# Kernel optimization log

Hardware: AMD Instinct MI355X
Metric: run time of the kernel (lower is better)

The kernel has to match this reference:

```python
import jax, jax.numpy as jnp
import numpy as np

B, N, DIM, H = 4, 2048, 256, 8
HD = DIM // H  # head_dim = 32
N_LAYERS = 2


def quantum_map(x):
    # cat over last dim: [cos(x+i*pi/2), sin(x+i*pi/2)] for i in 0..n_layers-1
    feats = []
    for i in range(N_LAYERS):
        phase = x + i * (np.pi / 2)
        feats.append(jnp.cos(phase))
        feats.append(jnp.sin(phase))
    return jnp.concatenate(feats, axis=-1)  # [..., 4*HD]


def setup_inputs() -> dict:
    key = jax.random.key(0)
    ks = jax.random.split(key, 10)
    s = 1.0 / np.sqrt(DIM)
    return {
        "x": jax.random.normal(ks[0], (B, N, DIM), dtype=jnp.float32),
        "topo_weights": jax.random.uniform(ks[1], (B, N, N), dtype=jnp.float32),
        "Wq": jax.random.normal(ks[2], (DIM, DIM), dtype=jnp.float32) * s,
        "bq": jnp.zeros((DIM,), jnp.float32),
        "Wk": jax.random.normal(ks[3], (DIM, DIM), dtype=jnp.float32) * s,
        "bk": jnp.zeros((DIM,), jnp.float32),
        "Wv": jax.random.normal(ks[4], (DIM, DIM), dtype=jnp.float32) * s,
        "bv": jnp.zeros((DIM,), jnp.float32),
        "Wo": jax.random.normal(ks[5], (DIM, DIM), dtype=jnp.float32) * s,
        "bo": jnp.zeros((DIM,), jnp.float32),
    }


def reference(x, topo_weights, Wq, bq, Wk, bk, Wv, bv, Wo, bo):
    b, n, c = x.shape
    q = (x @ Wq + bq).reshape(b, n, H, HD)
    k = (x @ Wk + bk).reshape(b, n, H, HD)
    v = (x @ Wv + bv).reshape(b, n, H, HD)
    q = quantum_map(q)  # [b,n,H,4*HD]
    k = quantum_map(k)
    scores = jnp.einsum('bnhd,bmhd->bnmh', q, k) / np.sqrt(HD)
    scores = scores * topo_weights[..., None]  # [b,n,m,h]
    attn = jax.nn.softmax(scores, axis=2)
    out = jnp.einsum('bnmh,bmhd->bnhd', attn, v).reshape(b, n, c)
    return out @ Wo + bo
```

## Files before the change

### kernel.cpp

```cpp
#include <hip/hip_runtime.h>
#include <math.h>

#define Bn 4
#define Nn 2048
#define Hn 8
#define HDn 32
#define Dn 256
#define MHALF 1024
#define NT 64

typedef _Float16 h1;
typedef __attribute__((ext_vector_type(2))) _Float16 h2;
typedef __attribute__((ext_vector_type(8))) _Float16 h8;
typedef __attribute__((ext_vector_type(4))) float fx4;

#define QSCALE 0.35355339059327373f
#define QS_L2E 0.5101185553493001f
#define SH_L2E 5.770780163555851f

__global__ __launch_bounds__(256) void cvtW_kernel(
    const float* __restrict__ Wq, const float* __restrict__ Wk,
    const float* __restrict__ Wv, const float* __restrict__ Wo,
    h1* __restrict__ WT)
{
    __shared__ float tw[64][65];
    const int w = blockIdx.z;
    const int d0 = blockIdx.y * 64, o0 = blockIdx.x * 64;
    const float* W = (w == 0) ? Wq : (w == 1) ? Wk : (w == 2) ? Wv : Wo;
    const int rr = threadIdx.x >> 6, cc = threadIdx.x & 63;
#pragma unroll
    for (int i = 0; i < 16; ++i)
        tw[rr + i * 4][cc] = W[(size_t)(d0 + rr + i * 4) * 256 + o0 + cc];
    __syncthreads();
#pragma unroll
    for (int i = 0; i < 16; ++i) {
        const int row = rr + i * 4;
        WT[(size_t)w * 65536 + (size_t)(o0 + row) * 256 + d0 + cc] = (h1)tw[cc][row];
    }
}

__global__ __launch_bounds__(256) __attribute__((amdgpu_waves_per_eu(4, 4)))
void proj_kernel(
    const float* __restrict__ x, const h1* __restrict__ WT,
    const float* __restrict__ bq, const float* __restrict__ bk,
    const float* __restrict__ bv,
    h1* __restrict__ fq, h1* __restrict__ fk, h1* __restrict__ vT)
{
    __shared__ __align__(16) h1 fbuf[64][264];
    const int tid = threadIdx.x;
    const int w = tid >> 6;
    const int lane = tid & 63;
    const int quad = lane >> 4;
    const int l15 = lane & 15;
    const int wsel = blockIdx.y >> 1;
    const int hg = blockIdx.y & 1;
    const int r0 = blockIdx.x * 64;
    const int arow = r0 + w * 16 + l15;
    const int b = r0 >> 11, n0 = r0 & (Nn - 1);

    const h1* WTw = WT + (size_t)wsel * 65536;
    fx4 acc[8];
#pragma unroll
    for (int ct = 0; ct < 8; ++ct) acc[ct] = (fx4){0.f, 0.f, 0.f, 0.f};

    for (int ks = 0; ks < 8; ++ks) {
        float xv[8];
        *(float4*)&xv[0] = *(const float4*)&x[(size_t)arow * 256 + ks * 32 + quad * 8];
        *(float4*)&xv[4] = *(const float4*)&x[(size_t)arow * 256 + ks * 32 + quad * 8 + 4];
        h8 Ahi, Alo;
#pragma unroll
        for (int j = 0; j < 8; ++j) {
            const h1 hi = (h1)xv[j];
            Ahi[j] = hi;
            Alo[j] = (h1)(xv[j] - (float)hi);
        }
        h8 Bf[8];
#pragma unroll
        for (int ct = 0; ct < 8; ++ct)
            Bf[ct] = *(const h8*)&WTw[(size_t)(hg * 128 + ct * 16 + l15) * 256 + ks * 32 + quad * 8];
#pragma unroll
        for (int ct = 0; ct < 8; ++ct) {
            acc[ct] = __builtin_amdgcn_mfma_f32_16x16x32_f16(Ahi, Bf[ct], acc[ct], 0, 0, 0);
            acc[ct] = __builtin_amdgcn_mfma_f32_16x16x32_f16(Alo, Bf[ct], acc[ct], 0, 0, 0);
        }
    }

    const float* bias = (wsel == 0) ? bq : (wsel == 1) ? bk : bv;

    if (wsel < 2) {
        h1* f = (wsel == 0) ? fq : fk;
#pragma unroll
        for (int ct = 0; ct < 8; ++ct) {
            const int c = ct * 16 + l15;
            const float bb = bias[hg * 128 + c];
            const int hh4 = c >> 5, dd = c & 31;
#pragma unroll
            for (int r = 0; r < 4; ++r) {
                const float val = acc[ct][r] + bb;
                const float sv = __sinf(val), cv = __cosf(val);
                h1* fp = &fbuf[w * 16 + quad * 4 + r][hh4 * 64 + dd];
                fp[0]  = (h1)cv;
                fp[32] = (h1)sv;
            }
        }
        __syncthreads();
        const int row = tid >> 2, q4 = tid & 3;
#pragma unroll
        for (int g = 0; g < 8; ++g) {
            const int chunk = q4 + g * 4;
            const int hh4 = chunk >> 3, within = chunk & 7;
            const h8 val = *(const h8*)&fbuf[row][hh4 * 64 + within * 8];
            const int head = hg * 4 + hh4;
            *(h8*)&f[((size_t)(b * Hn + head) * Nn + n0 + row) * 64 + within * 8] = val;
        }
    } else {
        h1 (*vst)[132] = (h1(*)[132])fbuf;
#pragma unroll
        for (int ct = 0; ct < 8; ++ct) {
            const int c = ct * 16 + l15;
            const float bb = bias[hg * 128 + c];
#pragma unroll
            for (int r = 0; r < 4; ++r)
                vst[w * 16 + quad * 4 + r][c] = (h1)(acc[ct][r] + bb);
        }
        __syncthreads();
        const int c2 = tid & 127, half = tid >> 7;
        const int head = hg * 4 + (c2 >> 5), dd = c2 & 31;
        h1* vp = vT + ((size_t)((b * Hn + head) * HDn + dd)) * Nn + n0;
#pragma unroll
        for (int g = 0; g < 4; ++g) {
            const int gg = half * 4 + g;
            h8 pk;
#pragma unroll
            for (int j = 0; j < 8; ++j) {
                const int zz = gg * 8 + j;
                const int blk = zz >> 5, z = zz & 31;
                const int src = blk * 32 + ((z & 7) >> 2) * 16 + (z >> 3) * 4 + (z & 3);
                pk[j] = vst[src][c2];
            }
            *(h8*)(vp + gg * 8) = pk;
        }
    }
}

__global__ __launch_bounds__(512, 1) void attn_kernel(
    const h1* __restrict__ fq, const h1* __restrict__ fk, const h1* __restrict__ vT,
    const float* __restrict__ topo, float* __restrict__ pacc, float* __restrict__ pl)
{
    __shared__ __align__(16) float tbuf[2][NT][40];

    const int b = blockIdx.y;
    const int mh = blockIdx.z;
    const int n0 = blockIdx.x * NT;
    const int tid = threadIdx.x;
    const int w = tid >> 6;
    const int h = w;
    const int lane = tid & 63;
    const int quad = lane >> 4;
    const int l15 = lane & 15;

    const h1* qfh = fq + (size_t)(b * Hn + h) * Nn * 64;
    const h1* kfh = fk + (size_t)(b * Hn + h) * Nn * 64;
    const h1* vTh = vT + (size_t)(b * Hn + h) * HDn * Nn;

    const int trow = tid >> 3, tcol4 = (tid & 7) * 4;
    const float* tpg = topo + (size_t)b * Nn * Nn + (size_t)(n0 + trow) * Nn + tcol4;

    h8 qfr[4][2];
#pragma unroll
    for (int qs = 0; qs < 4; ++qs)
#pragma unroll
        for (int ks = 0; ks < 2; ++ks)
            qfr[qs][ks] = *(const h8*)(qfh + (size_t)(n0 + qs * 16 + l15) * 64 + ks * 32 + quad * 8);

    fx4 acc[4][2];
    float lsum[4];
#pragma unroll
    for (int qs = 0; qs < 4; ++qs) {
#pragma unroll
        for (int ds = 0; ds < 2; ++ds) acc[qs][ds] = (fx4){0.f, 0.f, 0.f, 0.f};
        lsum[qs] = 0.f;
    }

    const int mbase = mh * MHALF;
    const fx4 z4 = {0.f, 0.f, 0.f, 0.f};

    float4 rt = *(const float4*)(tpg + mbase);

    for (int it = 0; it < MHALF / 32; ++it) {
        const int m0 = mbase + it * 32;
        const int cur = it & 1;

        h8 kfr[2][2];
#pragma unroll
        for (int ms = 0; ms < 2; ++ms)
#pragma unroll
            for (int ks = 0; ks < 2; ++ks)
                kfr[ms][ks] = *(const h8*)(kfh + (size_t)(m0 + ms * 16 + l15) * 64 + ks * 32 + quad * 8);
        h8 bV[2];
#pragma unroll
        for (int ds = 0; ds < 2; ++ds)
            bV[ds] = *(const h8*)(vTh + (size_t)(ds * 16 + l15) * Nn + m0 + quad * 8);

        *(float4*)&tbuf[cur][trow][tcol4] = rt;
        if (it < MHALF / 32 - 1) rt = *(const float4*)(tpg + m0 + 32);
        __asm__ volatile("s_waitcnt lgkmcnt(0)\n\ts_barrier" ::: "memory");

#pragma unroll
        for (int qs = 0; qs < 4; ++qs) {
            h2 pk[2][2];
#pragma unroll
            for (int ms = 0; ms < 2; ++ms) {
                fx4 tmp = __builtin_amdgcn_mfma_f32_16x16x32_f16(kfr[ms][0], qfr[qs][0], z4, 0, 0, 0);
                fx4 S2  = __builtin_amdgcn_mfma_f32_16x16x32_f16(kfr[ms][1], qfr[qs][1], tmp, 0, 0, 0);
                const fx4 tv = *(const fx4*)&tbuf[cur][qs * 16 + l15][ms * 16 + quad * 4];
                const float p0 = exp2f(fmaf(S2[0] * tv[0], QS_L2E, -SH_L2E));
                const float p1 = exp2f(fmaf(S2[1] * tv[1], QS_L2E, -SH_L2E));
                const float p2 = exp2f(fmaf(S2[2] * tv[2], QS_L2E, -SH_L2E));
                const float p3 = exp2f(fmaf(S2[3] * tv[3], QS_L2E, -SH_L2E));
                lsum[qs] += (p0 + p1) + (p2 + p3);
                pk[ms][0] = __builtin_bit_cast(h2, __builtin_amdgcn_cvt_pkrtz(p0, p1));
                pk[ms][1] = __builtin_bit_cast(h2, __builtin_amdgcn_cvt_pkrtz(p2, p3));
            }
            union { h8 v; h2 p[4]; } pa;
            pa.p[0] = pk[0][0]; pa.p[1] = pk[0][1];
            pa.p[2] = pk[1][0]; pa.p[3] = pk[1][1];
#pragma unroll
            for (int ds = 0; ds < 2; ++ds)
                acc[qs][ds] = __builtin_amdgcn_mfma_f32_16x16x32_f16(pa.v, bV[ds], acc[qs][ds], 0, 0, 0);
        }
    }

#pragma unroll
    for (int qs = 0; qs < 4; ++qs) {
        lsum[qs] += __shfl_xor(lsum[qs], 16);
        lsum[qs] += __shfl_xor(lsum[qs], 32);
    }

    float* paccm = pacc + (size_t)mh * Bn * Nn * Dn;
    float* plm   = pl   + (size_t)mh * Bn * Nn * Hn;
#pragma unroll
    for (int qs = 0; qs < 4; ++qs) {
#pragma unroll
        for (int r = 0; r < 4; ++r) {
            const size_t grow = (size_t)b * Nn + n0 + qs * 16 + quad * 4 + r;
            paccm[grow * Dn + h * HDn + l15]      = acc[qs][0][r];
            paccm[grow * Dn + h * HDn + 16 + l15] = acc[qs][1][r];
        }
        if (quad == 0)
            plm[((size_t)b * Nn + n0 + qs * 16 + l15) * Hn + h] = lsum[qs];
    }
}

__global__ __launch_bounds__(256) void oproj_kernel(
    const float* __restrict__ pacc, const float* __restrict__ pl,
    const h1* __restrict__ WoT, const float* __restrict__ bo,
    float* __restrict__ out)
{
    const int tid = threadIdx.x;
    const int w = tid >> 6;
    const int lane = tid & 63;
    const int quad = lane >> 4;
    const int l15 = lane & 15;
    const int r0 = blockIdx.x * 64;
    const int hg = blockIdx.y;
    const int arow = r0 + w * 16 + l15;
    const size_t PACC = (size_t)Bn * Nn * Dn;
    const size_t PL = (size_t)Bn * Nn * Hn;

    float rl[8];
#pragma unroll
    for (int hh = 0; hh < 8; ++hh) {
        const float l = pl[(size_t)arow * Hn + hh] + pl[PL + (size_t)arow * Hn + hh];
        rl[hh] = __builtin_amdgcn_rcpf(l);
    }

    fx4 acc[8];
#pragma unroll
    for (int ct = 0; ct < 8; ++ct) acc[ct] = (fx4){0.f, 0.f, 0.f, 0.f};

    for (int ks = 0; ks < 8; ++ks) {
        float a0[8], a1[8];
        const size_t base = (size_t)arow * Dn + ks * 32 + quad * 8;
        *(float4*)&a0[0] = *(const float4*)&pacc[base];
        *(float4*)&a0[4] = *(const float4*)&pacc[base + 4];
        *(float4*)&a1[0] = *(const float4*)&pacc[PACC + base];
        *(float4*)&a1[4] = *(const float4*)&pacc[PACC + base + 4];
        h8 Ahi, Alo;
#pragma unroll
        for (int j = 0; j < 8; ++j) {
            const float yv = (a0[j] + a1[j]) * rl[ks];
            const h1 hi = (h1)yv;
            Ahi[j] = hi;
            Alo[j] = (h1)(yv - (float)hi);
        }
        h8 Bf[8];
#pragma unroll
        for (int ct = 0; ct < 8; ++ct)
            Bf[ct] = *(const h8*)&WoT[(size_t)(hg * 128 + ct * 16 + l15) * 256 + ks * 32 + quad * 8];
#pragma unroll
        for (int ct = 0; ct < 8; ++ct) {
            acc[ct] = __builtin_amdgcn_mfma_f32_16x16x32_f16(Ahi, Bf[ct], acc[ct], 0, 0, 0);
            acc[ct] = __builtin_amdgcn_mfma_f32_16x16x32_f16(Alo, Bf[ct], acc[ct], 0, 0, 0);
        }
    }

#pragma unroll
    for (int ct = 0; ct < 8; ++ct) {
        const int col = hg * 128 + ct * 16 + l15;
        const float bb = bo[col];
#pragma unroll
        for (int r = 0; r < 4; ++r)
            out[(size_t)(r0 + w * 16 + quad * 4 + r) * 256 + col] = acc[ct][r] + bb;
    }
}

extern "C" void kernel_launch(void* const* d_in, const int* in_sizes, int n_in,
                              void* d_out, int out_size, void* d_ws, size_t ws_size,
                              hipStream_t stream)
{
    const float* x    = (const float*)d_in[0];
    const float* topo = (const float*)d_in[1];
    const float* Wq   = (const float*)d_in[2];
    const float* bq   = (const float*)d_in[3];
    const float* Wk   = (const float*)d_in[4];
    const float* bk   = (const float*)d_in[5];
    const float* Wv   = (const float*)d_in[6];
    const float* bv   = (const float*)d_in[7];
    const float* Wo   = (const float*)d_in[8];
    const float* bo   = (const float*)d_in[9];
    float* out = (float*)d_out;

    char* ws = (char*)d_ws;
    const size_t MB = 1024 * 1024;
    h1* WT = (h1*)ws;
    h1* fq = (h1*)(ws + 1 * MB);
    h1* fk = (h1*)(ws + 9 * MB);
    h1* vT = (h1*)(ws + 17 * MB);
    float* pacc = (float*)(ws + 21 * MB);
    float* pl   = (float*)(ws + 37 * MB);

    cvtW_kernel<<<dim3(4, 4, 4), 256, 0, stream>>>(Wq, Wk, Wv, Wo, WT);
    proj_kernel<<<dim3(128, 6), 256, 0, stream>>>(x, WT, bq, bk, bv, fq, fk, vT);
    attn_kernel<<<dim3(Nn / NT, Bn, 2), 512, 0, stream>>>(fq, fk, vT, topo, pacc, pl);
    oproj_kernel<<<dim3(128, 2), 256, 0, stream>>>(pacc, pl, WT + 3 * 65536, bo, out);
}
```

Before: 212.9 us.

## Split attention key range into four chunks and fold score scale into topo

Measured after the change: 232.7 us. 9.3% more time.

```diff
diff --git a/kernel.cpp b/kernel.cpp
--- a/kernel.cpp
+++ b/kernel.cpp
@@ -6,7 +6,7 @@
 #define Hn 8
 #define HDn 32
 #define Dn 256
-#define MHALF 1024
+#define MQ 512
 #define NT 64
 
 typedef _Float16 h1;
@@ -143,7 +143,7 @@
     }
 }
 
-__global__ __launch_bounds__(512, 1) void attn_kernel(
+__global__ __launch_bounds__(512, 2) void attn_kernel(
     const h1* __restrict__ fq, const h1* __restrict__ fk, const h1* __restrict__ vT,
     const float* __restrict__ topo, float* __restrict__ pacc, float* __restrict__ pl)
 {
@@ -182,12 +182,12 @@
         lsum[qs] = 0.f;
     }
 
-    const int mbase = mh * MHALF;
+    const int mbase = mh * MQ;
     const fx4 z4 = {0.f, 0.f, 0.f, 0.f};
 
     float4 rt = *(const float4*)(tpg + mbase);
 
-    for (int it = 0; it < MHALF / 32; ++it) {
+    for (int it = 0; it < MQ / 32; ++it) {
         const int m0 = mbase + it * 32;
         const int cur = it & 1;
 
@@ -202,8 +202,11 @@
         for (int ds = 0; ds < 2; ++ds)
             bV[ds] = *(const h8*)(vTh + (size_t)(ds * 16 + l15) * Nn + m0 + quad * 8);
 
-        *(float4*)&tbuf[cur][trow][tcol4] = rt;
-        if (it < MHALF / 32 - 1) rt = *(const float4*)(tpg + m0 + 32);
+        float4 rs;
+        rs.x = rt.x * QS_L2E; rs.y = rt.y * QS_L2E;
+        rs.z = rt.z * QS_L2E; rs.w = rt.w * QS_L2E;
+        *(float4*)&tbuf[cur][trow][tcol4] = rs;
+        if (it < MQ / 32 - 1) rt = *(const float4*)(tpg + m0 + 32);
         __asm__ volatile("s_waitcnt lgkmcnt(0)\n\ts_barrier" ::: "memory");
 
 #pragma unroll
@@ -214,10 +217,10 @@
                 fx4 tmp = __builtin_amdgcn_mfma_f32_16x16x32_f16(kfr[ms][0], qfr[qs][0], z4, 0, 0, 0);
                 fx4 S2  = __builtin_amdgcn_mfma_f32_16x16x32_f16(kfr[ms][1], qfr[qs][1], tmp, 0, 0, 0);
                 const fx4 tv = *(const fx4*)&tbuf[cur][qs * 16 + l15][ms * 16 + quad * 4];
-                const float p0 = exp2f(fmaf(S2[0] * tv[0], QS_L2E, -SH_L2E));
-                const float p1 = exp2f(fmaf(S2[1] * tv[1], QS_L2E, -SH_L2E));
-                const float p2 = exp2f(fmaf(S2[2] * tv[2], QS_L2E, -SH_L2E));
-                const float p3 = exp2f(fmaf(S2[3] * tv[3], QS_L2E, -SH_L2E));
+                const float p0 = exp2f(fmaf(S2[0], tv[0], -SH_L2E));
+                const float p1 = exp2f(fmaf(S2[1], tv[1], -SH_L2E));
+                const float p2 = exp2f(fmaf(S2[2], tv[2], -SH_L2E));
+                const float p3 = exp2f(fmaf(S2[3], tv[3], -SH_L2E));
                 lsum[qs] += (p0 + p1) + (p2 + p3);
                 pk[ms][0] = __builtin_bit_cast(h2, __builtin_amdgcn_cvt_pkrtz(p0, p1));
                 pk[ms][1] = __builtin_bit_cast(h2, __builtin_amdgcn_cvt_pkrtz(p2, p3));
@@ -271,7 +274,10 @@
     float rl[8];
 #pragma unroll
     for (int hh = 0; hh < 8; ++hh) {
-        const float l = pl[(size_t)arow * Hn + hh] + pl[PL + (size_t)arow * Hn + hh];
+        float l = 0.f;
+#pragma unroll
+        for (int m = 0; m < 4; ++m)
+            l += pl[m * PL + (size_t)arow * Hn + hh];
         rl[hh] = __builtin_amdgcn_rcpf(l);
     }
 
@@ -280,16 +286,21 @@
     for (int ct = 0; ct < 8; ++ct) acc[ct] = (fx4){0.f, 0.f, 0.f, 0.f};
 
     for (int ks = 0; ks < 8; ++ks) {
+        const size_t base = (size_t)arow * Dn + ks * 32 + quad * 8;
         float a0[8], a1[8];
-        const size_t base = (size_t)arow * Dn + ks * 32 + quad * 8;
         *(float4*)&a0[0] = *(const float4*)&pacc[base];
         *(float4*)&a0[4] = *(const float4*)&pacc[base + 4];
-        *(float4*)&a1[0] = *(const float4*)&pacc[PACC + base];
-        *(float4*)&a1[4] = *(const float4*)&pacc[PACC + base + 4];
+#pragma unroll
+        for (int m = 1; m < 4; ++m) {
+            *(float4*)&a1[0] = *(const float4*)&pacc[m * PACC + base];
+            *(float4*)&a1[4] = *(const float4*)&pacc[m * PACC + base + 4];
+#pragma unroll
+            for (int j = 0; j < 8; ++j) a0[j] += a1[j];
+        }
         h8 Ahi, Alo;
 #pragma unroll
         for (int j = 0; j < 8; ++j) {
-            const float yv = (a0[j] + a1[j]) * rl[ks];
+            const float yv = a0[j] * rl[ks];
             const h1 hi = (h1)yv;
             Ahi[j] = hi;
             Alo[j] = (h1)(yv - (float)hi);
@@ -338,10 +349,10 @@
     h1* fk = (h1*)(ws + 9 * MB);
     h1* vT = (h1*)(ws + 17 * MB);
     float* pacc = (float*)(ws + 21 * MB);
-    float* pl   = (float*)(ws + 37 * MB);
+    float* pl   = (float*)(ws + 53 * MB);
 
     cvtW_kernel<<<dim3(4, 4, 4), 256, 0, stream>>>(Wq, Wk, Wv, Wo, WT);
     proj_kernel<<<dim3(128, 6), 256, 0, stream>>>(x, WT, bq, bk, bv, fq, fk, vT);
-    attn_kernel<<<dim3(Nn / NT, Bn, 2), 512, 0, stream>>>(fq, fk, vT, topo, pacc, pl);
+    attn_kernel<<<dim3(Nn / NT, Bn, 4), 512, 0, stream>>>(fq, fk, vT, topo, pacc, pl);
     oproj_kernel<<<dim3(128, 2), 256, 0, stream>>>(pacc, pl, WT + 3 * 65536, bo, out);
 }
```
